# Kernel tuning notes

Hardware: AMD Instinct MI355X
Metric: run time of the kernel (lower is better)

## Reference

```python
import jax, jax.numpy as jnp
import numpy as np

B, N, C = 8, 4096, 1024
ATT_DIM = 512
M = 64  # num_outputs


def setup_inputs() -> dict:
    key = jax.random.key(0)
    k_x, k_w, k_b, k_av = jax.random.split(key, 4)
    x = jax.random.normal(k_x, (B, N, C), dtype=jnp.float32)
    # nn.Linear(input_dim, attention_dim): weight (att, C), bias (att,)
    lim = 1.0 / np.sqrt(C)
    W = jax.random.uniform(k_w, (ATT_DIM, C), dtype=jnp.float32, minval=-lim, maxval=lim)
    b = jax.random.uniform(k_b, (ATT_DIM,), dtype=jnp.float32, minval=-lim, maxval=lim)
    # torch.rand -> uniform [0,1)
    attention_vectors = jax.random.uniform(k_av, (M, ATT_DIM), dtype=jnp.float32)
    return {"x": x, "W": W, "b": b, "attention_vectors": attention_vectors}


def reference(x, W, b, attention_vectors):
    # linear projection: (B,N,C) @ (C,att) + bias -> (B,N,att)
    scores = jnp.einsum('bnc,dc->bnd', x, W) + b
    # learned-query attention logits: (B,M,N)
    logits = jnp.einsum('bnd,md->bmn', scores, attention_vectors)
    weights = jax.nn.softmax(logits, axis=-1)
    # pool original features: (B,M,N) @ (B,N,C) -> (B,M,C)
    return jnp.einsum('bmn,bnc->bmc', weights, x)
```

## Files before the change

### kernel.cpp

```cpp
#include <hip/hip_runtime.h>
#include <hip/hip_bf16.h>

#define Bn 8
#define Nn 4096
#define Cn 1024
#define Dn 512
#define Mn 64

typedef __hip_bfloat16 bf16;
typedef __attribute__((ext_vector_type(8))) short short8;
typedef __attribute__((ext_vector_type(4))) short short4x;
typedef __attribute__((ext_vector_type(4))) float f32x4;

#define MFMA16(a, b, c) __builtin_amdgcn_mfma_f32_16x16x32_bf16((a), (b), (c), 0, 0, 0)

__device__ inline short bfbits(float f) {
  union { bf16 b; short s; } u;
  u.b = __float2bfloat16(f);
  return u.s;
}

__global__ __launch_bounds__(256) void prep_kernel(
    const float* __restrict__ W, const float* __restrict__ bias,
    const float* __restrict__ av, bf16* __restrict__ Vhi,
    bf16* __restrict__ Vlo, float* __restrict__ c0) {
  const int m = blockIdx.x;
  const int t = threadIdx.x;
  const int cl = t & 63, dg = t >> 6;
  const int c = blockIdx.y * 64 + cl;
  const float* wp = W + (size_t)(dg * 128) * Cn + c;
  const float* ap = av + m * Dn + dg * 128;
  float a0 = 0.f, a1 = 0.f, a2 = 0.f, a3 = 0.f;
#pragma unroll 8
  for (int i = 0; i < 128; i += 4) {
    a0 = fmaf(ap[i + 0], wp[(size_t)(i + 0) * Cn], a0);
    a1 = fmaf(ap[i + 1], wp[(size_t)(i + 1) * Cn], a1);
    a2 = fmaf(ap[i + 2], wp[(size_t)(i + 2) * Cn], a2);
    a3 = fmaf(ap[i + 3], wp[(size_t)(i + 3) * Cn], a3);
  }
  __shared__ float red[256];
  red[t] = (a0 + a1) + (a2 + a3);
  __syncthreads();
  const float v = red[cl] + red[cl + 64] + red[cl + 128] + red[cl + 192];
  if (dg == 0) {
    const bf16 hi = __float2bfloat16(v);
    Vhi[m * Cn + c] = hi;
    Vlo[m * Cn + c] = __float2bfloat16(v - __bfloat162float(hi));
  }
  if (blockIdx.y == 0) {
    __syncthreads();
    red[t] = av[m * Dn + t] * bias[t] + av[m * Dn + t + 256] * bias[t + 256];
    __syncthreads();
    if (t < 64) {
      float s = red[t] + red[t + 64] + red[t + 128] + red[t + 192];
#pragma unroll
      for (int off = 32; off > 0; off >>= 1) s += __shfl_down(s, off);
      if (t == 0) c0[m] = s;
    }
  }
}

__global__ __launch_bounds__(256, 2) void logits_kernel(
    const float* __restrict__ x, const bf16* __restrict__ Vhi,
    const bf16* __restrict__ Vlo, const float* __restrict__ c0,
    float* __restrict__ logits) {
  const int n0 = blockIdx.x * 64;
  const int b = blockIdx.y;
  const int t = threadIdx.x;
  __shared__ short VsH[2][64][72];
  __shared__ short VsL[2][64][72];
  const int w = t >> 6, lane = t & 63, lr = lane & 15, q = lane >> 4;

  const float* xrow = x + (size_t)(b * Nn + n0 + w * 16 + lr) * Cn + q * 8;

  const int vr = t >> 3, vs = (t & 7) * 8;
  const bf16* vh0 = Vhi + (size_t)vr * Cn + vs;
  const bf16* vh1 = vh0 + (size_t)32 * Cn;
  const bf16* vl0 = Vlo + (size_t)vr * Cn + vs;
  const bf16* vl1 = vl0 + (size_t)32 * Cn;

  f32x4 acc[4];
#pragma unroll
  for (int i = 0; i < 4; ++i) acc[i] = (f32x4){0.f, 0.f, 0.f, 0.f};

  short8 ph0 = *(const short8*)(vh0);
  short8 ph1 = *(const short8*)(vh1);
  short8 pl0 = *(const short8*)(vl0);
  short8 pl1 = *(const short8*)(vl1);
  *(short8*)&VsH[0][vr][vs] = ph0;
  *(short8*)&VsH[0][vr + 32][vs] = ph1;
  *(short8*)&VsL[0][vr][vs] = pl0;
  *(short8*)&VsL[0][vr + 32][vs] = pl1;
  ph0 = *(const short8*)(vh0 + 64);
  ph1 = *(const short8*)(vh1 + 64);
  pl0 = *(const short8*)(vl0 + 64);
  pl1 = *(const short8*)(vl1 + 64);

  float4 xa0[2], xa1[2], xb0[2], xb1[2], xc0[2], xc1[2];
#pragma unroll
  for (int s = 0; s < 2; ++s) {
    xa0[s] = *(const float4*)(xrow + s * 32);
    xa1[s] = *(const float4*)(xrow + s * 32 + 4);
    xb0[s] = *(const float4*)(xrow + 64 + s * 32);
    xb1[s] = *(const float4*)(xrow + 64 + s * 32 + 4);
    xc0[s] = xb0[s]; xc1[s] = xb1[s];
  }

  int cur = 0;
  for (int kc = 0; kc < Cn; kc += 64, cur ^= 1) {
    __syncthreads();
    if (kc + 64 < Cn) {
      *(short8*)&VsH[cur ^ 1][vr][vs] = ph0;
      *(short8*)&VsH[cur ^ 1][vr + 32][vs] = ph1;
      *(short8*)&VsL[cur ^ 1][vr][vs] = pl0;
      *(short8*)&VsL[cur ^ 1][vr + 32][vs] = pl1;
      if (kc + 128 < Cn) {
        ph0 = *(const short8*)(vh0 + kc + 128);
        ph1 = *(const short8*)(vh1 + kc + 128);
        pl0 = *(const short8*)(vl0 + kc + 128);
        pl1 = *(const short8*)(vl1 + kc + 128);
      }
    }
    if (kc + 128 < Cn) {
#pragma unroll
      for (int s = 0; s < 2; ++s) {
        xc0[s] = *(const float4*)(xrow + kc + 128 + s * 32);
        xc1[s] = *(const float4*)(xrow + kc + 128 + s * 32 + 4);
      }
    }
#pragma unroll
    for (int s = 0; s < 2; ++s) {
      short8 a;
      a[0] = bfbits(xa0[s].x); a[1] = bfbits(xa0[s].y);
      a[2] = bfbits(xa0[s].z); a[3] = bfbits(xa0[s].w);
      a[4] = bfbits(xa1[s].x); a[5] = bfbits(xa1[s].y);
      a[6] = bfbits(xa1[s].z); a[7] = bfbits(xa1[s].w);
#pragma unroll
      for (int mt = 0; mt < 4; ++mt) {
        acc[mt] = MFMA16(a, *(const short8*)&VsH[cur][mt * 16 + lr][s * 32 + q * 8], acc[mt]);
        acc[mt] = MFMA16(a, *(const short8*)&VsL[cur][mt * 16 + lr][s * 32 + q * 8], acc[mt]);
      }
    }
#pragma unroll
    for (int s = 0; s < 2; ++s) {
      xa0[s] = xb0[s]; xa1[s] = xb1[s];
      xb0[s] = xc0[s]; xb1[s] = xc1[s];
    }
  }
#pragma unroll
  for (int mt = 0; mt < 4; ++mt) {
    const int m = mt * 16 + lr;
    const float bb = c0[m];
    float4 o;
    o.x = acc[mt][0] + bb; o.y = acc[mt][1] + bb;
    o.z = acc[mt][2] + bb; o.w = acc[mt][3] + bb;
    *(float4*)&logits[(size_t)(b * Mn + m) * Nn + n0 + w * 16 + q * 4] = o;
  }
}

__global__ __launch_bounds__(256) void softmax_kernel(
    const float* __restrict__ logits, bf16* __restrict__ wgt) {
  const int row = blockIdx.x;
  const int t = threadIdx.x;
  const float* L = logits + (size_t)row * Nn;
  float v[16];
  float mx = -3.4e38f;
#pragma unroll
  for (int i = 0; i < 16; ++i) {
    v[i] = L[t + 256 * i];
    mx = fmaxf(mx, v[i]);
  }
#pragma unroll
  for (int off = 32; off > 0; off >>= 1) mx = fmaxf(mx, __shfl_down(mx, off));
  __shared__ float sred[4];
  if ((t & 63) == 0) sred[t >> 6] = mx;
  __syncthreads();
  mx = fmaxf(fmaxf(sred[0], sred[1]), fmaxf(sred[2], sred[3]));
  float sum = 0.f;
#pragma unroll
  for (int i = 0; i < 16; ++i) {
    v[i] = __expf(v[i] - mx);
    sum += v[i];
  }
#pragma unroll
  for (int off = 32; off > 0; off >>= 1) sum += __shfl_down(sum, off);
  __syncthreads();
  if ((t & 63) == 0) sred[t >> 6] = sum;
  __syncthreads();
  const float inv = 1.f / (sred[0] + sred[1] + sred[2] + sred[3]);
#pragma unroll
  for (int i = 0; i < 16; ++i)
    wgt[(size_t)row * Nn + t + 256 * i] = __float2bfloat16(v[i] * inv);
}

__global__ __launch_bounds__(256, 4) void pool_kernel(
    const float* __restrict__ x, const bf16* __restrict__ wgt,
    float* __restrict__ part) {
  const int cbase = blockIdx.x * 64;
  const int b = blockIdx.y;
  const int ks = blockIdx.z;
  const int t = threadIdx.x;
  __shared__ short XT[2][64][136];
  const int w = t >> 6, lane = t & 63, lr = lane & 15, q = lane >> 4;
  const int mh = (w & 1) * 32, ch = (w >> 1) * 32;
  f32x4 acc[2][2];
#pragma unroll
  for (int i = 0; i < 2; ++i)
#pragma unroll
    for (int j = 0; j < 2; ++j) acc[i][j] = (f32x4){0.f, 0.f, 0.f, 0.f};

  const int h = t & 15, g = t >> 4;
  const int swz = 8 * (h & 7);
  const int swzr0 = 8 * (((ch + lr) >> 2) & 7);
  const int swzr1 = 8 * (((ch + 16 + lr) >> 2) & 7);
  const int NQ = Nn / 8;
  const int kbase = ks * NQ;
  const float* xsrc = x + (size_t)b * Nn * Cn + (size_t)(kbase + 4 * g) * Cn + cbase + 4 * h;
  const bf16* wr0 = wgt + (size_t)(b * Mn + mh + lr) * Nn + kbase;
  const bf16* wr1 = wr0 + (size_t)16 * Nn;

  float4 pf[8];
#pragma unroll
  for (int i = 0; i < 4; ++i) {
    pf[i]     = *(const float4*)(xsrc + (size_t)i * Cn);
    pf[4 + i] = *(const float4*)(xsrc + (size_t)(64 + i) * Cn);
  }
#pragma unroll
  for (int blk = 0; blk < 2; ++blk) {
    const float4 r0 = pf[blk * 4 + 0], r1 = pf[blk * 4 + 1];
    const float4 r2 = pf[blk * 4 + 2], r3 = pf[blk * 4 + 3];
    const int kof = (blk * 64 + 4 * g) ^ swz;
    short4x v0, v1, v2, v3;
    v0[0] = bfbits(r0.x); v0[1] = bfbits(r1.x); v0[2] = bfbits(r2.x); v0[3] = bfbits(r3.x);
    v1[0] = bfbits(r0.y); v1[1] = bfbits(r1.y); v1[2] = bfbits(r2.y); v1[3] = bfbits(r3.y);
    v2[0] = bfbits(r0.z); v2[1] = bfbits(r1.z); v2[2] = bfbits(r2.z); v2[3] = bfbits(r3.z);
    v3[0] = bfbits(r0.w); v3[1] = bfbits(r1.w); v3[2] = bfbits(r2.w); v3[3] = bfbits(r3.w);
    *(short4x*)&XT[0][4 * h + 0][kof] = v0;
    *(short4x*)&XT[0][4 * h + 1][kof] = v1;
    *(short4x*)&XT[0][4 * h + 2][kof] = v2;
    *(short4x*)&XT[0][4 * h + 3][kof] = v3;
  }
#pragma unroll
  for (int i = 0; i < 4; ++i) {
    pf[i]     = *(const float4*)(xsrc + (size_t)(128 + i) * Cn);
    pf[4 + i] = *(const float4*)(xsrc + (size_t)(192 + i) * Cn);
  }

  int cur = 0;
  for (int kc = 0; kc < NQ; kc += 128, cur ^= 1) {
    __syncthreads();
    if (kc + 128 < NQ) {
#pragma unroll
      for (int blk = 0; blk < 2; ++blk) {
        const float4 r0 = pf[blk * 4 + 0], r1 = pf[blk * 4 + 1];
        const float4 r2 = pf[blk * 4 + 2], r3 = pf[blk * 4 + 3];
        const int kof = (blk * 64 + 4 * g) ^ swz;
        short4x v0, v1, v2, v3;
        v0[0] = bfbits(r0.x); v0[1] = bfbits(r1.x); v0[2] = bfbits(r2.x); v0[3] = bfbits(r3.x);
        v1[0] = bfbits(r0.y); v1[1] = bfbits(r1.y); v1[2] = bfbits(r2.y); v1[3] = bfbits(r3.y);
        v2[0] = bfbits(r0.z); v2[1] = bfbits(r1.z); v2[2] = bfbits(r2.z); v2[3] = bfbits(r3.z);
        v3[0] = bfbits(r0.w); v3[1] = bfbits(r1.w); v3[2] = bfbits(r2.w); v3[3] = bfbits(r3.w);
        *(short4x*)&XT[cur ^ 1][4 * h + 0][kof] = v0;
        *(short4x*)&XT[cur ^ 1][4 * h + 1][kof] = v1;
        *(short4x*)&XT[cur ^ 1][4 * h + 2][kof] = v2;
        *(short4x*)&XT[cur ^ 1][4 * h + 3][kof] = v3;
      }
      if (kc + 256 < NQ) {
#pragma unroll
        for (int i = 0; i < 4; ++i) {
          pf[i]     = *(const float4*)(xsrc + (size_t)(kc + 256 + i) * Cn);
          pf[4 + i] = *(const float4*)(xsrc + (size_t)(kc + 320 + i) * Cn);
        }
      }
    }
#pragma unroll
    for (int kk = 0; kk < 128; kk += 32) {
      const short8 a0 = *(const short8*)(wr0 + kc + kk + q * 8);
      const short8 a1 = *(const short8*)(wr1 + kc + kk + q * 8);
      const short8 b0 = *(const short8*)&XT[cur][ch + lr][(kk + q * 8) ^ swzr0];
      const short8 b1 = *(const short8*)&XT[cur][ch + 16 + lr][(kk + q * 8) ^ swzr1];
      acc[0][0] = MFMA16(a0, b0, acc[0][0]);
      acc[0][1] = MFMA16(a0, b1, acc[0][1]);
      acc[1][0] = MFMA16(a1, b0, acc[1][0]);
      acc[1][1] = MFMA16(a1, b1, acc[1][1]);
    }
  }
  float* pout = part + ((size_t)ks * Bn + b) * Mn * Cn;
#pragma unroll
  for (int mi = 0; mi < 2; ++mi)
#pragma unroll
    for (int ci = 0; ci < 2; ++ci) {
      const int m = mh + mi * 16 + q * 4;
      const int c = cbase + ch + ci * 16 + lr;
#pragma unroll
      for (int reg = 0; reg < 4; ++reg)
        pout[(size_t)(m + reg) * Cn + c] = acc[mi][ci][reg];
    }
}

__global__ __launch_bounds__(256) void reduce_kernel(
    const float* __restrict__ part, float* __restrict__ out) {
  const int i = blockIdx.x * 256 + threadIdx.x;
  const float4* p = (const float4*)part;
  const int S4 = (Bn * Mn * Cn) / 4;
  float4 o = (float4){0.f, 0.f, 0.f, 0.f};
#pragma unroll
  for (int j = 0; j < 8; ++j) {
    const float4 v = p[i + j * S4];
    o.x += v.x; o.y += v.y; o.z += v.z; o.w += v.w;
  }
  ((float4*)out)[i] = o;
}

extern "C" void kernel_launch(void* const* d_in, const int* in_sizes, int n_in,
                              void* d_out, int out_size, void* d_ws, size_t ws_size,
                              hipStream_t stream) {
  const float* x = (const float*)d_in[0];
  const float* W = (const float*)d_in[1];
  const float* bias = (const float*)d_in[2];
  const float* av = (const float*)d_in[3];
  float* out = (float*)d_out;
  char* ws = (char*)d_ws;

  bf16* Vhi = (bf16*)(ws + 0);
  bf16* Vlo = (bf16*)(ws + 131072);
  float* c0 = (float*)(ws + 262144);
  bf16* wgt = (bf16*)(ws + 263168);
  float* logits = (float*)(ws + 4457472);
  float* part = (float*)(ws + 4457472);

  prep_kernel<<<dim3(Mn, Cn / 64), 256, 0, stream>>>(W, bias, av, Vhi, Vlo, c0);
  logits_kernel<<<dim3(Nn / 64, Bn), 256, 0, stream>>>(x, Vhi, Vlo, c0, logits);
  softmax_kernel<<<Bn * Mn, 256, 0, stream>>>(logits, wgt);
  pool_kernel<<<dim3(Cn / 64, Bn, 8), 256, 0, stream>>>(x, wgt, part);
  reduce_kernel<<<(Bn * Mn * Cn) / 1024, 256, 0, stream>>>(part, out);
}
```

Baseline: 254.8 us.

## Use direct global-to-LDS loads with pre-swizzled tile layouts for V and weights

The prep and softmax kernels now write V (hi/lo) and the softmax weights into pre-tiled, XOR-swizzled layouts. The logits and pool kernels can then stage them into LDS with global_load_lds, with no register round trip and no padding. The pool kernel also reads its weight operand from LDS instead of directly from global memory. It halves the split-K factor (8 to 4) and lowers occupancy to 2 to fit the larger LDS footprint, and the reduce kernel is adjusted to match. This trades fewer partial sums and cheaper staging for fewer blocks in flight in pool_kernel.

```diff
diff --git a/kernel.cpp b/kernel.cpp
--- a/kernel.cpp
+++ b/kernel.cpp
@@ -20,10 +20,16 @@
   return u.s;
 }
 
+__device__ __forceinline__ void gl_lds16(const bf16* g, short* l) {
+  __builtin_amdgcn_global_load_lds(
+      (const __attribute__((address_space(1))) void*)g,
+      (__attribute__((address_space(3))) void*)l, 16, 0, 0);
+}
+
 __global__ __launch_bounds__(256) void prep_kernel(
     const float* __restrict__ W, const float* __restrict__ bias,
-    const float* __restrict__ av, bf16* __restrict__ Vhi,
-    bf16* __restrict__ Vlo, float* __restrict__ c0) {
+    const float* __restrict__ av, bf16* __restrict__ VgH,
+    bf16* __restrict__ VgL, float* __restrict__ c0) {
   const int m = blockIdx.x;
   const int t = threadIdx.x;
   const int cl = t & 63, dg = t >> 6;
@@ -43,9 +49,10 @@
   __syncthreads();
   const float v = red[cl] + red[cl + 64] + red[cl + 128] + red[cl + 192];
   if (dg == 0) {
+    const int idx = blockIdx.y * 4096 + m * 64 + (cl ^ ((m & 7) << 3));
     const bf16 hi = __float2bfloat16(v);
-    Vhi[m * Cn + c] = hi;
-    Vlo[m * Cn + c] = __float2bfloat16(v - __bfloat162float(hi));
+    VgH[idx] = hi;
+    VgL[idx] = __float2bfloat16(v - __bfloat162float(hi));
   }
   if (blockIdx.y == 0) {
     __syncthreads();
@@ -61,40 +68,28 @@
 }
 
 __global__ __launch_bounds__(256, 2) void logits_kernel(
-    const float* __restrict__ x, const bf16* __restrict__ Vhi,
-    const bf16* __restrict__ Vlo, const float* __restrict__ c0,
+    const float* __restrict__ x, const bf16* __restrict__ VgH,
+    const bf16* __restrict__ VgL, const float* __restrict__ c0,
     float* __restrict__ logits) {
   const int n0 = blockIdx.x * 64;
   const int b = blockIdx.y;
   const int t = threadIdx.x;
-  __shared__ short VsH[2][64][72];
-  __shared__ short VsL[2][64][72];
+  __shared__ short VsH[2][4096];
+  __shared__ short VsL[2][4096];
   const int w = t >> 6, lane = t & 63, lr = lane & 15, q = lane >> 4;
 
   const float* xrow = x + (size_t)(b * Nn + n0 + w * 16 + lr) * Cn + q * 8;
 
-  const int vr = t >> 3, vs = (t & 7) * 8;
-  const bf16* vh0 = Vhi + (size_t)vr * Cn + vs;
-  const bf16* vh1 = vh0 + (size_t)32 * Cn;
-  const bf16* vl0 = Vlo + (size_t)vr * Cn + vs;
-  const bf16* vl1 = vl0 + (size_t)32 * Cn;
-
   f32x4 acc[4];
 #pragma unroll
   for (int i = 0; i < 4; ++i) acc[i] = (f32x4){0.f, 0.f, 0.f, 0.f};
 
-  short8 ph0 = *(const short8*)(vh0);
-  short8 ph1 = *(const short8*)(vh1);
-  short8 pl0 = *(const short8*)(vl0);
-  short8 pl1 = *(const short8*)(vl1);
-  *(short8*)&VsH[0][vr][vs] = ph0;
-  *(short8*)&VsH[0][vr + 32][vs] = ph1;
-  *(short8*)&VsL[0][vr][vs] = pl0;
-  *(short8*)&VsL[0][vr + 32][vs] = pl1;
-  ph0 = *(const short8*)(vh0 + 64);
-  ph1 = *(const short8*)(vh1 + 64);
-  pl0 = *(const short8*)(vl0 + 64);
-  pl1 = *(const short8*)(vl1 + 64);
+#pragma unroll
+  for (int r = 0; r < 2; ++r) {
+    const int off = (w + 4 * r) * 512;
+    gl_lds16(VgH + off + lane * 8, &VsH[0][off]);
+    gl_lds16(VgL + off + lane * 8, &VsL[0][off]);
+  }
 
   float4 xa0[2], xa1[2], xb0[2], xb1[2], xc0[2], xc1[2];
 #pragma unroll
@@ -106,21 +101,19 @@
     xc0[s] = xb0[s]; xc1[s] = xb1[s];
   }
 
+  const int rsw = (lr & 7) << 3;
   int cur = 0;
-  for (int kc = 0; kc < Cn; kc += 64, cur ^= 1) {
+  for (int ck = 0; ck < 16; ++ck, cur ^= 1) {
     __syncthreads();
-    if (kc + 64 < Cn) {
-      *(short8*)&VsH[cur ^ 1][vr][vs] = ph0;
-      *(short8*)&VsH[cur ^ 1][vr + 32][vs] = ph1;
-      *(short8*)&VsL[cur ^ 1][vr][vs] = pl0;
-      *(short8*)&VsL[cur ^ 1][vr + 32][vs] = pl1;
-      if (kc + 128 < Cn) {
-        ph0 = *(const short8*)(vh0 + kc + 128);
-        ph1 = *(const short8*)(vh1 + kc + 128);
-        pl0 = *(const short8*)(vl0 + kc + 128);
-        pl1 = *(const short8*)(vl1 + kc + 128);
-      }
-    }
+    if (ck + 1 < 16) {
+#pragma unroll
+      for (int r = 0; r < 2; ++r) {
+        const int off = (w + 4 * r) * 512;
+        gl_lds16(VgH + (ck + 1) * 4096 + off + lane * 8, &VsH[cur ^ 1][off]);
+        gl_lds16(VgL + (ck + 1) * 4096 + off + lane * 8, &VsL[cur ^ 1][off]);
+      }
+    }
+    const int kc = ck * 64;
     if (kc + 128 < Cn) {
 #pragma unroll
       for (int s = 0; s < 2; ++s) {
@@ -135,10 +128,12 @@
       a[2] = bfbits(xa0[s].z); a[3] = bfbits(xa0[s].w);
       a[4] = bfbits(xa1[s].x); a[5] = bfbits(xa1[s].y);
       a[6] = bfbits(xa1[s].z); a[7] = bfbits(xa1[s].w);
+      const int kx = (s * 32 + q * 8) ^ rsw;
 #pragma unroll
       for (int mt = 0; mt < 4; ++mt) {
-        acc[mt] = MFMA16(a, *(const short8*)&VsH[cur][mt * 16 + lr][s * 32 + q * 8], acc[mt]);
-        acc[mt] = MFMA16(a, *(const short8*)&VsL[cur][mt * 16 + lr][s * 32 + q * 8], acc[mt]);
+        const int idx = (mt * 16 + lr) * 64 + kx;
+        acc[mt] = MFMA16(a, *(const short8*)&VsH[cur][idx], acc[mt]);
+        acc[mt] = MFMA16(a, *(const short8*)&VsL[cur][idx], acc[mt]);
       }
     }
 #pragma unroll
@@ -161,6 +156,7 @@
 __global__ __launch_bounds__(256) void softmax_kernel(
     const float* __restrict__ logits, bf16* __restrict__ wgt) {
   const int row = blockIdx.x;
+  const int b = row >> 6, m = row & 63;
   const int t = threadIdx.x;
   const float* L = logits + (size_t)row * Nn;
   float v[16];
@@ -188,19 +184,24 @@
   if ((t & 63) == 0) sred[t >> 6] = sum;
   __syncthreads();
   const float inv = 1.f / (sred[0] + sred[1] + sred[2] + sred[3]);
-#pragma unroll
-  for (int i = 0; i < 16; ++i)
-    wgt[(size_t)row * Nn + t + 256 * i] = __float2bfloat16(v[i] * inv);
-}
-
-__global__ __launch_bounds__(256, 4) void pool_kernel(
+  const int msw = (m & 7) << 4;
+#pragma unroll
+  for (int i = 0; i < 16; ++i) {
+    const int n = t + 256 * i;
+    const int idx = (b * 32 + (n >> 7)) * 8192 + m * 128 + ((n & 127) ^ msw);
+    wgt[idx] = __float2bfloat16(v[i] * inv);
+  }
+}
+
+__global__ __launch_bounds__(256, 2) void pool_kernel(
     const float* __restrict__ x, const bf16* __restrict__ wgt,
     float* __restrict__ part) {
   const int cbase = blockIdx.x * 64;
   const int b = blockIdx.y;
   const int ks = blockIdx.z;
   const int t = threadIdx.x;
-  __shared__ short XT[2][64][136];
+  __shared__ short XT[2][64][128];
+  __shared__ short Ws[2][8192];
   const int w = t >> 6, lane = t & 63, lr = lane & 15, q = lane >> 4;
   const int mh = (w & 1) * 32, ch = (w >> 1) * 32;
   f32x4 acc[2][2];
@@ -210,14 +211,17 @@
     for (int j = 0; j < 2; ++j) acc[i][j] = (f32x4){0.f, 0.f, 0.f, 0.f};
 
   const int h = t & 15, g = t >> 4;
-  const int swz = 8 * (h & 7);
-  const int swzr0 = 8 * (((ch + lr) >> 2) & 7);
-  const int swzr1 = 8 * (((ch + 16 + lr) >> 2) & 7);
-  const int NQ = Nn / 8;
+  const int hb = 4 * (h & 1);
+  const int NQ = Nn / 4;
   const int kbase = ks * NQ;
+  const int tile0 = b * 32 + ks * 8;
   const float* xsrc = x + (size_t)b * Nn * Cn + (size_t)(kbase + 4 * g) * Cn + cbase + 4 * h;
-  const bf16* wr0 = wgt + (size_t)(b * Mn + mh + lr) * Nn + kbase;
-  const bf16* wr1 = wr0 + (size_t)16 * Nn;
+
+#pragma unroll
+  for (int r = 0; r < 4; ++r) {
+    const int off = (w + 4 * r) * 512;
+    gl_lds16(wgt + (size_t)tile0 * 8192 + off + lane * 8, &Ws[0][off]);
+  }
 
   float4 pf[8];
 #pragma unroll
@@ -229,16 +233,16 @@
   for (int blk = 0; blk < 2; ++blk) {
     const float4 r0 = pf[blk * 4 + 0], r1 = pf[blk * 4 + 1];
     const float4 r2 = pf[blk * 4 + 2], r3 = pf[blk * 4 + 3];
-    const int kof = (blk * 64 + 4 * g) ^ swz;
+    const int kb2 = blk * 64 + 4 * g;
     short4x v0, v1, v2, v3;
     v0[0] = bfbits(r0.x); v0[1] = bfbits(r1.x); v0[2] = bfbits(r2.x); v0[3] = bfbits(r3.x);
     v1[0] = bfbits(r0.y); v1[1] = bfbits(r1.y); v1[2] = bfbits(r2.y); v1[3] = bfbits(r3.y);
     v2[0] = bfbits(r0.z); v2[1] = bfbits(r1.z); v2[2] = bfbits(r2.z); v2[3] = bfbits(r3.z);
     v3[0] = bfbits(r0.w); v3[1] = bfbits(r1.w); v3[2] = bfbits(r2.w); v3[3] = bfbits(r3.w);
-    *(short4x*)&XT[0][4 * h + 0][kof] = v0;
-    *(short4x*)&XT[0][4 * h + 1][kof] = v1;
-    *(short4x*)&XT[0][4 * h + 2][kof] = v2;
-    *(short4x*)&XT[0][4 * h + 3][kof] = v3;
+    *(short4x*)&XT[0][4 * h + 0][kb2 ^ ((hb + 0) << 4)] = v0;
+    *(short4x*)&XT[0][4 * h + 1][kb2 ^ ((hb + 1) << 4)] = v1;
+    *(short4x*)&XT[0][4 * h + 2][kb2 ^ ((hb + 2) << 4)] = v2;
+    *(short4x*)&XT[0][4 * h + 3][kb2 ^ ((hb + 3) << 4)] = v3;
   }
 #pragma unroll
   for (int i = 0; i < 4; ++i) {
@@ -246,24 +250,31 @@
     pf[4 + i] = *(const float4*)(xsrc + (size_t)(192 + i) * Cn);
   }
 
+  const int asw = (lr & 7) << 4;
   int cur = 0;
   for (int kc = 0; kc < NQ; kc += 128, cur ^= 1) {
     __syncthreads();
     if (kc + 128 < NQ) {
 #pragma unroll
+      for (int r = 0; r < 4; ++r) {
+        const int off = (w + 4 * r) * 512;
+        gl_lds16(wgt + (size_t)(tile0 + (kc >> 7) + 1) * 8192 + off + lane * 8,
+                 &Ws[cur ^ 1][off]);
+      }
+#pragma unroll
       for (int blk = 0; blk < 2; ++blk) {
         const float4 r0 = pf[blk * 4 + 0], r1 = pf[blk * 4 + 1];
         const float4 r2 = pf[blk * 4 + 2], r3 = pf[blk * 4 + 3];
-        const int kof = (blk * 64 + 4 * g) ^ swz;
+        const int kb2 = blk * 64 + 4 * g;
         short4x v0, v1, v2, v3;
         v0[0] = bfbits(r0.x); v0[1] = bfbits(r1.x); v0[2] = bfbits(r2.x); v0[3] = bfbits(r3.x);
         v1[0] = bfbits(r0.y); v1[1] = bfbits(r1.y); v1[2] = bfbits(r2.y); v1[3] = bfbits(r3.y);
         v2[0] = bfbits(r0.z); v2[1] = bfbits(r1.z); v2[2] = bfbits(r2.z); v2[3] = bfbits(r3.z);
         v3[0] = bfbits(r0.w); v3[1] = bfbits(r1.w); v3[2] = bfbits(r2.w); v3[3] = bfbits(r3.w);
-        *(short4x*)&XT[cur ^ 1][4 * h + 0][kof] = v0;
-        *(short4x*)&XT[cur ^ 1][4 * h + 1][kof] = v1;
-        *(short4x*)&XT[cur ^ 1][4 * h + 2][kof] = v2;
-        *(short4x*)&XT[cur ^ 1][4 * h + 3][kof] = v3;
+        *(short4x*)&XT[cur ^ 1][4 * h + 0][kb2 ^ ((hb + 0) << 4)] = v0;
+        *(short4x*)&XT[cur ^ 1][4 * h + 1][kb2 ^ ((hb + 1) << 4)] = v1;
+        *(short4x*)&XT[cur ^ 1][4 * h + 2][kb2 ^ ((hb + 2) << 4)] = v2;
+        *(short4x*)&XT[cur ^ 1][4 * h + 3][kb2 ^ ((hb + 3) << 4)] = v3;
       }
       if (kc + 256 < NQ) {
 #pragma unroll
@@ -275,10 +286,11 @@
     }
 #pragma unroll
     for (int kk = 0; kk < 128; kk += 32) {
-      const short8 a0 = *(const short8*)(wr0 + kc + kk + q * 8);
-      const short8 a1 = *(const short8*)(wr1 + kc + kk + q * 8);
-      const short8 b0 = *(const short8*)&XT[cur][ch + lr][(kk + q * 8) ^ swzr0];
-      const short8 b1 = *(const short8*)&XT[cur][ch + 16 + lr][(kk + q * 8) ^ swzr1];
+      const int kx = (kk + q * 8) ^ asw;
+      const short8 a0 = *(const short8*)&Ws[cur][(mh + lr) * 128 + kx];
+      const short8 a1 = *(const short8*)&Ws[cur][(mh + 16 + lr) * 128 + kx];
+      const short8 b0 = *(const short8*)&XT[cur][ch + lr][kx];
+      const short8 b1 = *(const short8*)&XT[cur][ch + 16 + lr][kx];
       acc[0][0] = MFMA16(a0, b0, acc[0][0]);
       acc[0][1] = MFMA16(a0, b1, acc[0][1]);
       acc[1][0] = MFMA16(a1, b0, acc[1][0]);
@@ -305,7 +317,7 @@
   const int S4 = (Bn * Mn * Cn) / 4;
   float4 o = (float4){0.f, 0.f, 0.f, 0.f};
 #pragma unroll
-  for (int j = 0; j < 8; ++j) {
+  for (int j = 0; j < 4; ++j) {
     const float4 v = p[i + j * S4];
     o.x += v.x; o.y += v.y; o.z += v.z; o.w += v.w;
   }
@@ -322,16 +334,16 @@
   float* out = (float*)d_out;
   char* ws = (char*)d_ws;
 
-  bf16* Vhi = (bf16*)(ws + 0);
-  bf16* Vlo = (bf16*)(ws + 131072);
+  bf16* VgH = (bf16*)(ws + 0);
+  bf16* VgL = (bf16*)(ws + 131072);
   float* c0 = (float*)(ws + 262144);
   bf16* wgt = (bf16*)(ws + 263168);
   float* logits = (float*)(ws + 4457472);
   float* part = (float*)(ws + 4457472);
 
-  prep_kernel<<<dim3(Mn, Cn / 64), 256, 0, stream>>>(W, bias, av, Vhi, Vlo, c0);
-  logits_kernel<<<dim3(Nn / 64, Bn), 256, 0, stream>>>(x, Vhi, Vlo, c0, logits);
+  prep_kernel<<<dim3(Mn, Cn / 64), 256, 0, stream>>>(W, bias, av, VgH, VgL, c0);
+  logits_kernel<<<dim3(Nn / 64, Bn), 256, 0, stream>>>(x, VgH, VgL, c0, logits);
   softmax_kernel<<<Bn * Mn, 256, 0, stream>>>(logits, wgt);
-  pool_kernel<<<dim3(Cn / 64, Bn, 8), 256, 0, stream>>>(x, wgt, part);
+  pool_kernel<<<dim3(Cn / 64, Bn, 4), 256, 0, stream>>>(x, wgt, part);
   reduce_kernel<<<(Bn * Mn * Cn) / 1024, 256, 0, stream>>>(part, out);
 }
```

Measured after the change: 256.3 us. Within noise of the previous version (+0.6%).
